# Optimization experiments

Measured on AMD Instinct MI355X. Metric: run time of the kernel, lower is better.

Reference implementation:

```python
import jax, jax.numpy as jnp
import numpy as np

B, IN_C, OUT_C, NUM, DIM = 4096, 512, 512, 16, 128

def _unif(k, shape, fan_in):
    b = 1.0 / np.sqrt(fan_in)
    return jax.random.uniform(k, shape, jnp.float32, -b, b)

def setup_inputs() -> dict:
    key = jax.random.key(0)
    ks = jax.random.split(key, 9)
    inp = jax.random.normal(ks[0], (B, IN_C), jnp.float32)
    Wpre = _unif(ks[1], (DIM, IN_C), IN_C)        # nn.Linear weight (out, in)
    bpre = _unif(ks[2], (DIM,), IN_C)
    W = _unif(ks[3], (NUM, NUM, DIM, DIM), DIM)    # W[i,j] = link[i][j].weight (out=e, in=d)
    bl = _unif(ks[4], (NUM, NUM, DIM), DIM)        # link biases
    life = jax.random.uniform(ks[5], (NUM, NUM), jnp.float32) + 0.5  # rand(1)+0.5
    Wpost = _unif(ks[6], (OUT_C, DIM), DIM)
    bpost = _unif(ks[7], (OUT_C,), DIM)
    return {"inp": inp, "Wpre": Wpre, "bpre": bpre, "W": W, "b": bl,
            "life": life, "Wpost": Wpost, "bpost": bpost, "steps": 10}

def reference(inp, Wpre, bpre, W, b, life, Wpost, bpost, steps):
    num = life.shape[0]
    x = inp @ Wpre.T + bpre                         # [B, dim]
    gate = jnp.where(life > 0, life, 0.0)           # life>0 branch with scalar gain
    Wg = gate[:, :, None, None] * W                 # [num, num, dim, dim]
    bias = jnp.einsum('ij,ijd->jd', gate, b)        # per-step constant bias sum over i
    m0 = jnp.zeros((num,) + x.shape, x.dtype).at[0].set(x)  # matrix[0] = inp
    def step(m, _):
        # new[j] = sum_i gate[i,j] * (m[i] @ W[i,j].T + b[i,j])
        new = jnp.einsum('ibd,ijed->jbe', m, Wg) + bias[:, None, :]
        return new, None
    mT, _ = jax.lax.scan(step, m0, None, length=steps)
    return mT[num - 1] @ Wpost.T + bpost            # [B, out_c]
```

## Files before the change

### kernel.cpp

```cpp
#include <hip/hip_runtime.h>


typedef __bf16 bf16x8 __attribute__((ext_vector_type(8)));
typedef float f32x4 __attribute__((ext_vector_type(4)));
typedef __attribute__((address_space(3))) unsigned int lds_u32;
typedef const __attribute__((address_space(1))) unsigned int glb_u32;

__device__ __forceinline__ unsigned short f2bf(float x) {
  unsigned int u = __float_as_uint(x);
  u += 0x7FFFu + ((u >> 16) & 1u);
  return (unsigned short)(u >> 16);
}
__device__ __forceinline__ float bf2f(unsigned short s) {
  return __uint_as_float(((unsigned int)s) << 16);
}
__device__ __forceinline__ bf16x8 ldg8(const unsigned short* p) {
  return __builtin_bit_cast(bf16x8, *(const uint4*)p);
}
__device__ __forceinline__ f32x4 mfma16(bf16x8 a, bf16x8 b, f32x4 c) {
  return __builtin_amdgcn_mfma_f32_16x16x32_bf16(a, b, c, 0, 0, 0);
}

#define ND 2048
#define MT 144
#define KS 8
#define CKS 16

__global__ __launch_bounds__(256) void build_all(
    const float* __restrict__ W, const float* __restrict__ life,
    const float* __restrict__ bl, const float* __restrict__ inp,
    unsigned short* __restrict__ Ahi, unsigned short* __restrict__ Alo,
    unsigned short* __restrict__ Qhi, unsigned short* __restrict__ Qlo,
    unsigned short* __restrict__ Rhi, unsigned short* __restrict__ Rlo,
    float* __restrict__ beta,
    unsigned short* __restrict__ Ihi, unsigned short* __restrict__ Ilo) {
  const int tid = blockIdx.x * 256 + threadIdx.x;
  const int NT = gridDim.x * 256;

  for (int item = tid; item < (ND * ND) / 8; item += NT) {
    int base = item * 8;
    int n = base >> 11, k = base & 2047;
    int j = n >> 7, i = k >> 7;
    float gval = life[i * 16 + j];
    float gate = gval > 0.f ? gval : 0.f;
    const float* src = W + ((i * 16 + j) * 16384 + (n & 127) * 128 + (k & 127));
    float4 x = *(const float4*)src, y = *(const float4*)(src + 4);
    float vals[8] = {x.x, x.y, x.z, x.w, y.x, y.y, y.z, y.w};
    union { unsigned short u[8]; uint4 v; } ph, pl;
#pragma unroll
    for (int q = 0; q < 8; ++q) {
      float v = gate * vals[q];
      unsigned short h = f2bf(v);
      ph.u[q] = h;
      pl.u[q] = f2bf(v - bf2f(h));
    }
    *(uint4*)(Ahi + base) = ph.v;
    *(uint4*)(Alo + base) = pl.v;
  }

  for (int item = tid; item < MT * ND; item += NT) {
    int m = item >> 11, n = item & 2047;
    int j = n >> 7, e = n & 127;
    unsigned short hh = 0, ll = 0;
    if (m < 128) {
      float gval = life[j];
      float gate = gval > 0.f ? gval : 0.f;
      float v = gate * W[j * 16384 + e * 128 + m];
      hh = f2bf(v); ll = f2bf(v - bf2f(hh));
    } else if (m == 128) {
      float s = 0.f;
#pragma unroll
      for (int i = 0; i < 16; ++i) {
        float gval = life[i * 16 + j];
        float gate = gval > 0.f ? gval : 0.f;
        s += gate * bl[(i * 16 + j) * 128 + e];
      }
      beta[n] = s;
      hh = f2bf(s); ll = f2bf(s - bf2f(hh));
    }
    Qhi[item] = hh;
    Qlo[item] = ll;
  }

  for (int item = tid; item < MT * ND; item += NT) {
    int m = item >> 11, n = item & 2047;
    int i = n >> 7, d = n & 127;
    unsigned short hh = 0, ll = 0;
    if (m < 128) {
      float gval = life[i * 16 + 15];
      float gate = gval > 0.f ? gval : 0.f;
      float v = gate * W[(i * 16 + 15) * 16384 + m * 128 + d];
      hh = f2bf(v); ll = f2bf(v - bf2f(hh));
    }
    Rhi[item] = hh;
    Rlo[item] = ll;
  }

  for (int item = tid; item < (4096 * 512) / 8; item += NT) {
    int base = item * 8;
    float4 x = *(const float4*)(inp + base), y = *(const float4*)(inp + base + 4);
    float vals[8] = {x.x, x.y, x.z, x.w, y.x, y.y, y.z, y.w};
    union { unsigned short u[8]; uint4 v; } ph, pl;
#pragma unroll
    for (int q = 0; q < 8; ++q) {
      unsigned short h = f2bf(vals[q]);
      ph.u[q] = h;
      pl.u[q] = f2bf(vals[q] - bf2f(h));
    }
    *(uint4*)(Ihi + base) = ph.v;
    *(uint4*)(Ilo + base) = pl.v;
  }
}

__global__ __launch_bounds__(256) void build_AT(
    const unsigned short* __restrict__ Ahi, const unsigned short* __restrict__ Alo,
    unsigned short* __restrict__ AThi, unsigned short* __restrict__ ATlo) {
  __shared__ unsigned short Th[32][36], Tl[32][36];
  const int t = threadIdx.x;
  const int tx = blockIdx.x & 63;
  const int ty = blockIdx.x >> 6;
  const int r = t >> 3;
  const int c4 = (t & 7) * 4;
  union { uint2 d; unsigned short u[4]; } vh, vl;
  vh.d = *(const uint2*)(Ahi + (size_t)(tx * 32 + r) * ND + ty * 32 + c4);
  vl.d = *(const uint2*)(Alo + (size_t)(tx * 32 + r) * ND + ty * 32 + c4);
#pragma unroll
  for (int i = 0; i < 4; ++i) { Th[r][c4 + i] = vh.u[i]; Tl[r][c4 + i] = vl.u[i]; }
  __syncthreads();
  union { uint2 d; unsigned short u[4]; } oh, ol;
#pragma unroll
  for (int i = 0; i < 4; ++i) { oh.u[i] = Th[c4 + i][r]; ol.u[i] = Tl[c4 + i][r]; }
  *(uint2*)(AThi + (size_t)(ty * 32 + r) * ND + tx * 32 + c4) = oh.d;
  *(uint2*)(ATlo + (size_t)(ty * 32 + r) * ND + tx * 32 + c4) = ol.d;
}

__global__ __launch_bounds__(192, 2) void step_pair(
    const unsigned short* __restrict__ Ahi, const unsigned short* __restrict__ Alo,
    const unsigned short* __restrict__ AThi, const unsigned short* __restrict__ ATlo,
    const unsigned short* __restrict__ Qqhi, const unsigned short* __restrict__ Qqlo,
    const unsigned short* __restrict__ Qrhi, const unsigned short* __restrict__ Qrlo,
    float* __restrict__ Pq, float* __restrict__ Pr) {
  __shared__ __align__(16) unsigned short AS[64][256];
  const int t = threadIdx.x;
  const int g = t >> 6, lane = t & 63;
  const int r16 = lane & 15, q = lane >> 4;
  const int kc = blockIdx.x;
  const int nb = blockIdx.y;
  const int chain = blockIdx.z;
  const unsigned short* Bh = chain ? AThi : Ahi;
  const unsigned short* Bl = chain ? ATlo : Alo;
  const unsigned short* Qh = chain ? Qrhi : Qqhi;
  const unsigned short* Ql = chain ? Qrlo : Qqlo;
  float* P = chain ? Pr : Pq;
  const int kbase = kc * 256;
  const int n0 = nb * 32;

  for (int ch = g; ch < 32; ch += 3) {
    int s = ch * 64 + lane;
    int row = s >> 5;
    int c16 = (s & 31) ^ (row & 7);
    const unsigned short* src =
        (row < 32 ? Bh + (size_t)(n0 + row) * ND
                  : Bl + (size_t)(n0 + row - 32) * ND) + kbase + c16 * 8;
    __builtin_amdgcn_global_load_lds((glb_u32*)src,
                                     (lds_u32*)(&AS[0][0] + ch * 512), 16, 0, 0);
  }

  const int m0 = g * 48 + r16;
  const unsigned short* pA0h = Qh + (size_t)m0 * ND + kbase + q * 8;
  const unsigned short* pA0l = Ql + (size_t)m0 * ND + kbase + q * 8;

  bf16x8 qa[2][6];
#pragma unroll
  for (int f = 0; f < 3; ++f) {
    qa[0][2 * f]     = ldg8(pA0h + f * 16 * ND);
    qa[0][2 * f + 1] = ldg8(pA0l + f * 16 * ND);
  }
  __syncthreads();

  const uint4* ASv = (const uint4*)&AS[0][0];

  f32x4 acc[3][2];
#pragma unroll
  for (int mt = 0; mt < 3; ++mt)
#pragma unroll
    for (int nt = 0; nt < 2; ++nt) acc[mt][nt] = (f32x4){0.f, 0.f, 0.f, 0.f};

#pragma unroll
  for (int it = 0; it < 8; ++it) {
    const int cur = it & 1, nxt = cur ^ 1;
    if (it < 7) {
      const int ko = (it + 1) * 32;
#pragma unroll
      for (int f = 0; f < 3; ++f) {
        qa[nxt][2 * f]     = ldg8(pA0h + f * 16 * ND + ko);
        qa[nxt][2 * f + 1] = ldg8(pA0l + f * 16 * ND + ko);
      }
    }
    const int cx = (it * 4 + q) ^ (r16 & 7);
    bf16x8 b0h = __builtin_bit_cast(bf16x8, ASv[r16 * 32 + cx]);
    bf16x8 b1h = __builtin_bit_cast(bf16x8, ASv[(16 + r16) * 32 + cx]);
    bf16x8 b0l = __builtin_bit_cast(bf16x8, ASv[(32 + r16) * 32 + cx]);
    bf16x8 b1l = __builtin_bit_cast(bf16x8, ASv[(48 + r16) * 32 + cx]);

    acc[0][0] = mfma16(qa[cur][0], b0h, acc[0][0]);
    acc[0][0] = mfma16(qa[cur][1], b0h, acc[0][0]);
    acc[0][0] = mfma16(qa[cur][0], b0l, acc[0][0]);
    acc[1][0] = mfma16(qa[cur][2], b0h, acc[1][0]);
    acc[1][0] = mfma16(qa[cur][3], b0h, acc[1][0]);
    acc[1][0] = mfma16(qa[cur][2], b0l, acc[1][0]);
    acc[2][0] = mfma16(qa[cur][4], b0h, acc[2][0]);
    acc[2][0] = mfma16(qa[cur][5], b0h, acc[2][0]);
    acc[2][0] = mfma16(qa[cur][4], b0l, acc[2][0]);
    acc[0][1] = mfma16(qa[cur][0], b1h, acc[0][1]);
    acc[0][1] = mfma16(qa[cur][1], b1h, acc[0][1]);
    acc[0][1] = mfma16(qa[cur][0], b1l, acc[0][1]);
    acc[1][1] = mfma16(qa[cur][2], b1h, acc[1][1]);
    acc[1][1] = mfma16(qa[cur][3], b1h, acc[1][1]);
    acc[1][1] = mfma16(qa[cur][2], b1l, acc[1][1]);
    acc[2][1] = mfma16(qa[cur][4], b1h, acc[2][1]);
    acc[2][1] = mfma16(qa[cur][5], b1h, acc[2][1]);
    acc[2][1] = mfma16(qa[cur][4], b1l, acc[2][1]);
  }

  float* Pk = P + kc * (MT * ND);
#pragma unroll
  for (int mt = 0; mt < 3; ++mt)
#pragma unroll
    for (int nt = 0; nt < 2; ++nt) {
      int mbase = g * 48 + mt * 16 + q * 4;
      int n = n0 + nt * 16 + r16;
#pragma unroll
      for (int r = 0; r < 4; ++r)
        Pk[(mbase + r) * ND + n] = acc[mt][nt][r];
    }
}

__global__ __launch_bounds__(256) void reduce_pair(
    const float* __restrict__ Pq, const float* __restrict__ Pr,
    const float* __restrict__ beta,
    unsigned short* __restrict__ Oqh, unsigned short* __restrict__ Oql,
    unsigned short* __restrict__ Orh, unsigned short* __restrict__ Orl) {
  int bid = blockIdx.x;
  int chain = bid >= 288;
  int t = (bid - (chain ? 288 : 0)) * 256 + threadIdx.x;
  const float* P = chain ? Pr : Pq;
  unsigned short* Oh = chain ? Orh : Oqh;
  unsigned short* Ol = chain ? Orl : Oql;
  int m = t >> 9;
  int n = (t & 511) * 4;
  int idx = m * ND + n;
  const int stride = MT * ND;
  float v0 = 0.f, v1 = 0.f, v2 = 0.f, v3 = 0.f;
#pragma unroll
  for (int c = 0; c < KS; ++c) {
    float4 s = *(const float4*)(P + c * stride + idx);
    v0 += s.x; v1 += s.y; v2 += s.z; v3 += s.w;
  }
  if (!chain && m == 128) {
    float4 b4 = *(const float4*)(beta + n);
    v0 += b4.x; v1 += b4.y; v2 += b4.z; v3 += b4.w;
  }
  union { unsigned short u[4]; uint2 d; } h, l;
  float vv[4] = {v0, v1, v2, v3};
#pragma unroll
  for (int i = 0; i < 4; ++i) {
    unsigned short hh = f2bf(vv[i]);
    h.u[i] = hh;
    l.u[i] = f2bf(vv[i] - bf2f(hh));
  }
  *(uint2*)(Oh + idx) = h.d;
  *(uint2*)(Ol + idx) = l.d;
}

__global__ __launch_bounds__(192, 2) void contract_S(
    const unsigned short* __restrict__ R5h, const unsigned short* __restrict__ R5l,
    const unsigned short* __restrict__ Q5h, const unsigned short* __restrict__ Q5l,
    float* __restrict__ CP) {
  __shared__ __align__(16) unsigned short AS[64][128];
  const int t = threadIdx.x;
  const int g = t >> 6, lane = t & 63;
  const int r16 = lane & 15, q = lane >> 4;
  const int kc = blockIdx.x;
  const int nb = blockIdx.y;
  const int kbase = kc * 128;
  const int n0 = nb * 32;

  for (int ch = g; ch < 16; ch += 3) {
    int s = ch * 64 + lane;
    int row = s >> 4;
    int c16 = (s & 15) ^ (row & 7);
    const unsigned short* src =
        (row < 32 ? R5h + (size_t)(n0 + row) * ND
                  : R5l + (size_t)(n0 + row - 32) * ND) + kbase + c16 * 8;
    __builtin_amdgcn_global_load_lds((glb_u32*)src,
                                     (lds_u32*)(&AS[0][0] + ch * 512), 16, 0, 0);
  }

  const int m0 = g * 48 + r16;
  const unsigned short* pA0h = Q5h + (size_t)m0 * ND + kbase + q * 8;
  const unsigned short* pA0l = Q5l + (size_t)m0 * ND + kbase + q * 8;

  bf16x8 qa[2][6];
#pragma unroll
  for (int f = 0; f < 3; ++f) {
    qa[0][2 * f]     = ldg8(pA0h + f * 16 * ND);
    qa[0][2 * f + 1] = ldg8(pA0l + f * 16 * ND);
  }
  __syncthreads();

  const uint4* ASv = (const uint4*)&AS[0][0];

  f32x4 acc[3][2];
#pragma unroll
  for (int mt = 0; mt < 3; ++mt)
#pragma unroll
    for (int nt = 0; nt < 2; ++nt) acc[mt][nt] = (f32x4){0.f, 0.f, 0.f, 0.f};

#pragma unroll
  for (int it = 0; it < 4; ++it) {
    const int cur = it & 1, nxt = cur ^ 1;
    if (it < 3) {
      const int ko = (it + 1) * 32;
#pragma unroll
      for (int f = 0; f < 3; ++f) {
        qa[nxt][2 * f]     = ldg8(pA0h + f * 16 * ND + ko);
        qa[nxt][2 * f + 1] = ldg8(pA0l + f * 16 * ND + ko);
      }
    }
    const int cx = (it * 4 + q) ^ (r16 & 7);
    bf16x8 b0h = __builtin_bit_cast(bf16x8, ASv[r16 * 16 + cx]);
    bf16x8 b1h = __builtin_bit_cast(bf16x8, ASv[(16 + r16) * 16 + cx]);
    bf16x8 b0l = __builtin_bit_cast(bf16x8, ASv[(32 + r16) * 16 + cx]);
    bf16x8 b1l = __builtin_bit_cast(bf16x8, ASv[(48 + r16) * 16 + cx]);

    acc[0][0] = mfma16(qa[cur][0], b0h, acc[0][0]);
    acc[0][0] = mfma16(qa[cur][1], b0h, acc[0][0]);
    acc[0][0] = mfma16(qa[cur][0], b0l, acc[0][0]);
    acc[1][0] = mfma16(qa[cur][2], b0h, acc[1][0]);
    acc[1][0] = mfma16(qa[cur][3], b0h, acc[1][0]);
    acc[1][0] = mfma16(qa[cur][2], b0l, acc[1][0]);
    acc[2][0] = mfma16(qa[cur][4], b0h, acc[2][0]);
    acc[2][0] = mfma16(qa[cur][5], b0h, acc[2][0]);
    acc[2][0] = mfma16(qa[cur][4], b0l, acc[2][0]);
    acc[0][1] = mfma16(qa[cur][0], b1h, acc[0][1]);
    acc[0][1] = mfma16(qa[cur][1], b1h, acc[0][1]);
    acc[0][1] = mfma16(qa[cur][0], b1l, acc[0][1]);
    acc[1][1] = mfma16(qa[cur][2], b1h, acc[1][1]);
    acc[1][1] = mfma16(qa[cur][3], b1h, acc[1][1]);
    acc[1][1] = mfma16(qa[cur][2], b1l, acc[1][1]);
    acc[2][1] = mfma16(qa[cur][4], b1h, acc[2][1]);
    acc[2][1] = mfma16(qa[cur][5], b1h, acc[2][1]);
    acc[2][1] = mfma16(qa[cur][4], b1l, acc[2][1]);
  }

  float* Pk = CP + kc * (MT * 128);
#pragma unroll
  for (int mt = 0; mt < 3; ++mt)
#pragma unroll
    for (int nt = 0; nt < 2; ++nt) {
      int mbase = g * 48 + mt * 16 + q * 4;
      int n = n0 + nt * 16 + r16;
#pragma unroll
      for (int r = 0; r < 4; ++r)
        Pk[(mbase + r) * 128 + n] = acc[mt][nt][r];
    }
}

__global__ __launch_bounds__(256) void extract_Sc(
    const float* __restrict__ CP,
    const unsigned short* __restrict__ Q5h, const unsigned short* __restrict__ Q5l,
    float* __restrict__ St, float* __restrict__ gv) {
  int t = blockIdx.x * 256 + threadIdx.x;
  const int PSTR = MT * 128;
  if (t < 16384) {
    int d = t >> 7, e = t & 127;
    float v = 0.f;
#pragma unroll
    for (int c = 0; c < CKS; ++c) v += CP[c * PSTR + d * 128 + e];
    St[t] = v;
  } else if (t < 16512) {
    int e = t - 16384;
    float v = bf2f(Q5h[128 * ND + 1920 + e]) + bf2f(Q5l[128 * ND + 1920 + e]);
#pragma unroll
    for (int c = 0; c < CKS; ++c) v += CP[c * PSTR + 128 * 128 + e];
    gv[e] = v;
  }
}

__global__ __launch_bounds__(256) void tail_T1g(
    const float* __restrict__ St, const float* __restrict__ Wpre,
    const float* __restrict__ bpre, float* __restrict__ T1,
    float* __restrict__ gv) {
  int t = blockIdx.x * 256 + threadIdx.x;
  if (t < 65536) {
    int e = t >> 9, ic = t & 511;
    float s = 0.f;
    for (int d = 0; d < 128; ++d) s += St[d * 128 + e] * Wpre[d * 512 + ic];
    T1[t] = s;
  } else if (t < 65664) {
    int e = t - 65536;
    float s = gv[e];
    for (int d = 0; d < 128; ++d) s += St[d * 128 + e] * bpre[d];
    gv[e] = s;
  }
}

__global__ __launch_bounds__(256) void tail_Weff(
    const float* __restrict__ Wpost, const float* __restrict__ T1,
    const float* __restrict__ gv, const float* __restrict__ bpost,
    unsigned short* __restrict__ Whi, unsigned short* __restrict__ Wlo,
    float* __restrict__ beff) {
  int t = blockIdx.x * 256 + threadIdx.x;
  if (t < 262144) {
    int o = t >> 9, ic = t & 511;
    float s = 0.f;
    for (int e = 0; e < 128; ++e) s += Wpost[o * 128 + e] * T1[e * 512 + ic];
    unsigned short h = f2bf(s);
    Whi[t] = h;
    Wlo[t] = f2bf(s - bf2f(h));
  } else if (t < 262656) {
    int o = t - 262144;
    float s = bpost[o];
    for (int e = 0; e < 128; ++e) s += Wpost[o * 128 + e] * gv[e];
    beff[o] = s;
  }
}

__global__ __launch_bounds__(256) void final_gemm(
    const unsigned short* __restrict__ Ihi, const unsigned short* __restrict__ Ilo,
    const unsigned short* __restrict__ Whi, const unsigned short* __restrict__ Wlo,
    const float* __restrict__ beff, float* __restrict__ out) {
  __shared__ __align__(16) unsigned short Is_hi[64][40], Is_lo[64][40];
  __shared__ __align__(16) unsigned short Ws_hi[128][40], Ws_lo[128][40];
  const int t = threadIdx.x;
  const int mb = blockIdx.x, nb = blockIdx.y;
  const int w = t >> 6, lane = t & 63;
  const int r16 = lane & 15, q = lane >> 4;

  f32x4 acc[4][2];
#pragma unroll
  for (int x = 0; x < 4; ++x)
#pragma unroll
    for (int b = 0; b < 2; ++b) acc[x][b] = (f32x4){0.f, 0.f, 0.f, 0.f};

  for (int kc = 0; kc < 16; ++kc) {
    const int k0 = kc * 32;
#pragma unroll
    for (int rpt = 0; rpt < 6; ++rpt) {
      int slot = t + rpt * 256;
      if (slot < 512) {
        int arr = slot >> 8, s = slot & 255;
        int row = s >> 2, off = (s & 3) * 8;
        const unsigned short* src = arr ? Ilo : Ihi;
        unsigned short* dst = arr ? &Is_lo[row][off] : &Is_hi[row][off];
        *(uint4*)dst = *(const uint4*)(src + (mb * 64 + row) * 512 + k0 + off);
      } else {
        int s = slot - 512;
        int arr = s >> 9, s2 = s & 511;
        int row = s2 >> 2, off = (s2 & 3) * 8;
        const unsigned short* src = arr ? Wlo : Whi;
        unsigned short* dst = arr ? &Ws_lo[row][off] : &Ws_hi[row][off];
        *(uint4*)dst = *(const uint4*)(src + (nb * 128 + row) * 512 + k0 + off);
      }
    }
    __syncthreads();

    bf16x8 bh0 = __builtin_bit_cast(bf16x8, *(const uint4*)&Ws_hi[w * 32 + r16][q * 8]);
    bf16x8 bl0 = __builtin_bit_cast(bf16x8, *(const uint4*)&Ws_lo[w * 32 + r16][q * 8]);
    bf16x8 bh1 = __builtin_bit_cast(bf16x8, *(const uint4*)&Ws_hi[w * 32 + 16 + r16][q * 8]);
    bf16x8 bl1 = __builtin_bit_cast(bf16x8, *(const uint4*)&Ws_lo[w * 32 + 16 + r16][q * 8]);
#pragma unroll
    for (int mt = 0; mt < 4; ++mt) {
      bf16x8 ah = __builtin_bit_cast(bf16x8, *(const uint4*)&Is_hi[mt * 16 + r16][q * 8]);
      bf16x8 al = __builtin_bit_cast(bf16x8, *(const uint4*)&Is_lo[mt * 16 + r16][q * 8]);
      acc[mt][0] = mfma16(ah, bh0, acc[mt][0]);
      acc[mt][0] = mfma16(al, bh0, acc[mt][0]);
      acc[mt][0] = mfma16(ah, bl0, acc[mt][0]);
      acc[mt][1] = mfma16(ah, bh1, acc[mt][1]);
      acc[mt][1] = mfma16(al, bh1, acc[mt][1]);
      acc[mt][1] = mfma16(ah, bl1, acc[mt][1]);
    }
    __syncthreads();
  }

#pragma unroll
  for (int mt = 0; mt < 4; ++mt)
#pragma unroll
    for (int nt = 0; nt < 2; ++nt) {
      int n = nb * 128 + w * 32 + nt * 16 + r16;
      float bv = beff[n];
#pragma unroll
      for (int r = 0; r < 4; ++r) {
        int m = mb * 64 + mt * 16 + q * 4 + r;
        out[m * 512 + n] = acc[mt][nt][r] + bv;
      }
    }
}

extern "C" void kernel_launch(void* const* d_in, const int* in_sizes, int n_in,
                              void* d_out, int out_size, void* d_ws, size_t ws_size,
                              hipStream_t stream) {
  const float* inp   = (const float*)d_in[0];
  const float* Wpre  = (const float*)d_in[1];
  const float* bpre  = (const float*)d_in[2];
  const float* W     = (const float*)d_in[3];
  const float* bl    = (const float*)d_in[4];
  const float* life  = (const float*)d_in[5];
  const float* Wpost = (const float*)d_in[6];
  const float* bpost = (const float*)d_in[7];
  float* out = (float*)d_out;

  char* p = (char*)d_ws;
  auto alloc = [&](size_t bytes) {
    char* r = p;
    p += (bytes + 255) & ~(size_t)255;
    return r;
  };
  unsigned short* Ahi  = (unsigned short*)alloc((size_t)ND * ND * 2);
  unsigned short* Alo  = (unsigned short*)alloc((size_t)ND * ND * 2);
  unsigned short* AThi = (unsigned short*)alloc((size_t)ND * ND * 2);
  unsigned short* ATlo = (unsigned short*)alloc((size_t)ND * ND * 2);
  unsigned short* QqAh = (unsigned short*)alloc((size_t)MT * ND * 2);
  unsigned short* QqAl = (unsigned short*)alloc((size_t)MT * ND * 2);
  unsigned short* QqBh = (unsigned short*)alloc((size_t)MT * ND * 2);
  unsigned short* QqBl = (unsigned short*)alloc((size_t)MT * ND * 2);
  unsigned short* QrAh = (unsigned short*)alloc((size_t)MT * ND * 2);
  unsigned short* QrAl = (unsigned short*)alloc((size_t)MT * ND * 2);
  unsigned short* QrBh = (unsigned short*)alloc((size_t)MT * ND * 2);
  unsigned short* QrBl = (unsigned short*)alloc((size_t)MT * ND * 2);
  float* beta = (float*)alloc(ND * 4);
  float* Pq   = (float*)alloc((size_t)KS * MT * ND * 4);
  float* Pr   = (float*)alloc((size_t)KS * MT * ND * 4);
  float* CP   = (float*)alloc((size_t)CKS * MT * 128 * 4);
  float* St   = (float*)alloc(128 * 128 * 4);
  float* gv   = (float*)alloc(128 * 4);
  float* T1   = (float*)alloc(128 * 512 * 4);
  float* beff = (float*)alloc(512 * 4);
  unsigned short* Whi = (unsigned short*)alloc(512 * 512 * 2);
  unsigned short* Wlo = (unsigned short*)alloc(512 * 512 * 2);
  unsigned short* Ihi = (unsigned short*)alloc((size_t)4096 * 512 * 2);
  unsigned short* Ilo = (unsigned short*)alloc((size_t)4096 * 512 * 2);

  build_all<<<1024, 256, 0, stream>>>(W, life, bl, inp, Ahi, Alo,
                                      QqAh, QqAl, QrAh, QrAl, beta, Ihi, Ilo);
  build_AT<<<4096, 256, 0, stream>>>(Ahi, Alo, AThi, ATlo);

  const unsigned short *qqh = QqAh, *qql = QqAl, *qrh = QrAh, *qrl = QrAl;
  unsigned short *oqh = QqBh, *oql = QqBl, *orh = QrBh, *orl = QrBl;
  for (int s = 0; s < 4; ++s) {
    step_pair<<<dim3(KS, 64, 2), 192, 0, stream>>>(
        Ahi, Alo, AThi, ATlo, qqh, qql, qrh, qrl, Pq, Pr);
    reduce_pair<<<576, 256, 0, stream>>>(Pq, Pr, beta, oqh, oql, orh, orl);
    const unsigned short* t1 = qqh; qqh = oqh; oqh = (unsigned short*)t1;
    const unsigned short* t2 = qql; qql = oql; oql = (unsigned short*)t2;
    const unsigned short* t3 = qrh; qrh = orh; orh = (unsigned short*)t3;
    const unsigned short* t4 = qrl; qrl = orl; orl = (unsigned short*)t4;
  }

  contract_S<<<dim3(CKS, 4), 192, 0, stream>>>(qrh, qrl, qqh, qql, CP);
  extract_Sc<<<65, 256, 0, stream>>>(CP, qqh, qql, St, gv);
  tail_T1g<<<257, 256, 0, stream>>>(St, Wpre, bpre, T1, gv);
  tail_Weff<<<1026, 256, 0, stream>>>(Wpost, T1, gv, bpost, Whi, Wlo, beff);
  final_gemm<<<dim3(64, 4), 256, 0, stream>>>(Ihi, Ilo, Whi, Wlo, beff, out);
}
```

Before: 254.0 us.

## Fuse A transpose into build kernel and double-buffer final GEMM LDS tiles

The separate build_AT kernel is removed. build_all now produces both A and its transpose from the same register values through a shared-memory tile, so the second pass that re-read A from global memory and the extra launch disappear. Separately, final_gemm stages the next K chunk in registers while the current chunk is being multiplied, using double-buffered LDS so global loads overlap with MFMA work. The cost is more LDS and register pressure in final_gemm and extra block-wide barriers inside build_all's tile loop.

```diff
diff --git a/kernel.cpp b/kernel.cpp
--- a/kernel.cpp
+++ b/kernel.cpp
@@ -30,32 +30,49 @@
     const float* __restrict__ W, const float* __restrict__ life,
     const float* __restrict__ bl, const float* __restrict__ inp,
     unsigned short* __restrict__ Ahi, unsigned short* __restrict__ Alo,
+    unsigned short* __restrict__ AThi, unsigned short* __restrict__ ATlo,
     unsigned short* __restrict__ Qhi, unsigned short* __restrict__ Qlo,
     unsigned short* __restrict__ Rhi, unsigned short* __restrict__ Rlo,
     float* __restrict__ beta,
     unsigned short* __restrict__ Ihi, unsigned short* __restrict__ Ilo) {
+  __shared__ unsigned short Th[32][36], Tl[32][36];
   const int tid = blockIdx.x * 256 + threadIdx.x;
   const int NT = gridDim.x * 256;
-
-  for (int item = tid; item < (ND * ND) / 8; item += NT) {
-    int base = item * 8;
-    int n = base >> 11, k = base & 2047;
-    int j = n >> 7, i = k >> 7;
-    float gval = life[i * 16 + j];
-    float gate = gval > 0.f ? gval : 0.f;
-    const float* src = W + ((i * 16 + j) * 16384 + (n & 127) * 128 + (k & 127));
-    float4 x = *(const float4*)src, y = *(const float4*)(src + 4);
-    float vals[8] = {x.x, x.y, x.z, x.w, y.x, y.y, y.z, y.w};
-    union { unsigned short u[8]; uint4 v; } ph, pl;
-#pragma unroll
-    for (int q = 0; q < 8; ++q) {
-      float v = gate * vals[q];
-      unsigned short h = f2bf(v);
-      ph.u[q] = h;
-      pl.u[q] = f2bf(v - bf2f(h));
-    }
-    *(uint4*)(Ahi + base) = ph.v;
-    *(uint4*)(Alo + base) = pl.v;
+  const int t = threadIdx.x;
+
+  {
+    const int r = t >> 3;
+    const int c4 = (t & 7) * 4;
+    for (int tt = blockIdx.x; tt < 4096; tt += gridDim.x) {
+      int nt = tt & 63, kt = tt >> 6;
+      int j = nt >> 2, e0 = (nt & 3) * 32;
+      int i = kt >> 2, d0 = (kt & 3) * 32;
+      float gval = life[i * 16 + j];
+      float gate = gval > 0.f ? gval : 0.f;
+      const float* src = W + ((size_t)(i * 16 + j) * 16384 + (e0 + r) * 128 + d0 + c4);
+      float4 v = *(const float4*)src;
+      float vals[4] = {v.x, v.y, v.z, v.w};
+      union { unsigned short u[4]; uint2 d2; } oh, ol;
+#pragma unroll
+      for (int x = 0; x < 4; ++x) {
+        float s = gate * vals[x];
+        oh.u[x] = f2bf(s);
+        ol.u[x] = f2bf(s - bf2f(oh.u[x]));
+      }
+      size_t aidx = (size_t)(j * 128 + e0 + r) * ND + i * 128 + d0 + c4;
+      *(uint2*)(Ahi + aidx) = oh.d2;
+      *(uint2*)(Alo + aidx) = ol.d2;
+      __syncthreads();
+#pragma unroll
+      for (int x = 0; x < 4; ++x) { Th[r][c4 + x] = oh.u[x]; Tl[r][c4 + x] = ol.u[x]; }
+      __syncthreads();
+      union { unsigned short u[4]; uint2 d2; } th, tl;
+#pragma unroll
+      for (int x = 0; x < 4; ++x) { th.u[x] = Th[c4 + x][r]; tl.u[x] = Tl[c4 + x][r]; }
+      size_t tidx = (size_t)(i * 128 + d0 + r) * ND + j * 128 + e0 + c4;
+      *(uint2*)(AThi + tidx) = th.d2;
+      *(uint2*)(ATlo + tidx) = tl.d2;
+    }
   }
 
   for (int item = tid; item < MT * ND; item += NT) {
@@ -89,7 +106,7 @@
     if (m < 128) {
       float gval = life[i * 16 + 15];
       float gate = gval > 0.f ? gval : 0.f;
-      float v = gate * W[(i * 16 + 15) * 16384 + m * 128 + d];
+      float v = gate * W[(size_t)(i * 16 + 15) * 16384 + m * 128 + d];
       hh = f2bf(v); ll = f2bf(v - bf2f(hh));
     }
     Rhi[item] = hh;
@@ -110,28 +127,6 @@
     *(uint4*)(Ihi + base) = ph.v;
     *(uint4*)(Ilo + base) = pl.v;
   }
-}
-
-__global__ __launch_bounds__(256) void build_AT(
-    const unsigned short* __restrict__ Ahi, const unsigned short* __restrict__ Alo,
-    unsigned short* __restrict__ AThi, unsigned short* __restrict__ ATlo) {
-  __shared__ unsigned short Th[32][36], Tl[32][36];
-  const int t = threadIdx.x;
-  const int tx = blockIdx.x & 63;
-  const int ty = blockIdx.x >> 6;
-  const int r = t >> 3;
-  const int c4 = (t & 7) * 4;
-  union { uint2 d; unsigned short u[4]; } vh, vl;
-  vh.d = *(const uint2*)(Ahi + (size_t)(tx * 32 + r) * ND + ty * 32 + c4);
-  vl.d = *(const uint2*)(Alo + (size_t)(tx * 32 + r) * ND + ty * 32 + c4);
-#pragma unroll
-  for (int i = 0; i < 4; ++i) { Th[r][c4 + i] = vh.u[i]; Tl[r][c4 + i] = vl.u[i]; }
-  __syncthreads();
-  union { uint2 d; unsigned short u[4]; } oh, ol;
-#pragma unroll
-  for (int i = 0; i < 4; ++i) { oh.u[i] = Th[c4 + i][r]; ol.u[i] = Tl[c4 + i][r]; }
-  *(uint2*)(AThi + (size_t)(ty * 32 + r) * ND + tx * 32 + c4) = oh.d;
-  *(uint2*)(ATlo + (size_t)(ty * 32 + r) * ND + tx * 32 + c4) = ol.d;
 }
 
 __global__ __launch_bounds__(192, 2) void step_pair(
@@ -431,20 +426,15 @@
     const unsigned short* __restrict__ Ihi, const unsigned short* __restrict__ Ilo,
     const unsigned short* __restrict__ Whi, const unsigned short* __restrict__ Wlo,
     const float* __restrict__ beff, float* __restrict__ out) {
-  __shared__ __align__(16) unsigned short Is_hi[64][40], Is_lo[64][40];
-  __shared__ __align__(16) unsigned short Ws_hi[128][40], Ws_lo[128][40];
+  __shared__ __align__(16) unsigned short Is_hi[2][64][40], Is_lo[2][64][40];
+  __shared__ __align__(16) unsigned short Ws_hi[2][128][40], Ws_lo[2][128][40];
   const int t = threadIdx.x;
   const int mb = blockIdx.x, nb = blockIdx.y;
   const int w = t >> 6, lane = t & 63;
   const int r16 = lane & 15, q = lane >> 4;
 
-  f32x4 acc[4][2];
-#pragma unroll
-  for (int x = 0; x < 4; ++x)
-#pragma unroll
-    for (int b = 0; b < 2; ++b) acc[x][b] = (f32x4){0.f, 0.f, 0.f, 0.f};
-
-  for (int kc = 0; kc < 16; ++kc) {
+  uint4 stg[6];
+  auto load_regs = [&](int kc) {
     const int k0 = kc * 32;
 #pragma unroll
     for (int rpt = 0; rpt < 6; ++rpt) {
@@ -453,27 +443,57 @@
         int arr = slot >> 8, s = slot & 255;
         int row = s >> 2, off = (s & 3) * 8;
         const unsigned short* src = arr ? Ilo : Ihi;
-        unsigned short* dst = arr ? &Is_lo[row][off] : &Is_hi[row][off];
-        *(uint4*)dst = *(const uint4*)(src + (mb * 64 + row) * 512 + k0 + off);
+        stg[rpt] = *(const uint4*)(src + (mb * 64 + row) * 512 + k0 + off);
       } else {
         int s = slot - 512;
         int arr = s >> 9, s2 = s & 511;
         int row = s2 >> 2, off = (s2 & 3) * 8;
         const unsigned short* src = arr ? Wlo : Whi;
-        unsigned short* dst = arr ? &Ws_lo[row][off] : &Ws_hi[row][off];
-        *(uint4*)dst = *(const uint4*)(src + (nb * 128 + row) * 512 + k0 + off);
-      }
-    }
-    __syncthreads();
-
-    bf16x8 bh0 = __builtin_bit_cast(bf16x8, *(const uint4*)&Ws_hi[w * 32 + r16][q * 8]);
-    bf16x8 bl0 = __builtin_bit_cast(bf16x8, *(const uint4*)&Ws_lo[w * 32 + r16][q * 8]);
-    bf16x8 bh1 = __builtin_bit_cast(bf16x8, *(const uint4*)&Ws_hi[w * 32 + 16 + r16][q * 8]);
-    bf16x8 bl1 = __builtin_bit_cast(bf16x8, *(const uint4*)&Ws_lo[w * 32 + 16 + r16][q * 8]);
+        stg[rpt] = *(const uint4*)(src + (nb * 128 + row) * 512 + k0 + off);
+      }
+    }
+  };
+  auto store_lds = [&](int b) {
+#pragma unroll
+    for (int rpt = 0; rpt < 6; ++rpt) {
+      int slot = t + rpt * 256;
+      if (slot < 512) {
+        int arr = slot >> 8, s = slot & 255;
+        int row = s >> 2, off = (s & 3) * 8;
+        unsigned short* dst = arr ? &Is_lo[b][row][off] : &Is_hi[b][row][off];
+        *(uint4*)dst = stg[rpt];
+      } else {
+        int s = slot - 512;
+        int arr = s >> 9, s2 = s & 511;
+        int row = s2 >> 2, off = (s2 & 3) * 8;
+        unsigned short* dst = arr ? &Ws_lo[b][row][off] : &Ws_hi[b][row][off];
+        *(uint4*)dst = stg[rpt];
+      }
+    }
+  };
+
+  f32x4 acc[4][2];
+#pragma unroll
+  for (int x = 0; x < 4; ++x)
+#pragma unroll
+    for (int b = 0; b < 2; ++b) acc[x][b] = (f32x4){0.f, 0.f, 0.f, 0.f};
+
+  load_regs(0);
+  store_lds(0);
+  __syncthreads();
+
+  for (int kc = 0; kc < 16; ++kc) {
+    const int cur = kc & 1;
+    if (kc < 15) load_regs(kc + 1);
+
+    bf16x8 bh0 = __builtin_bit_cast(bf16x8, *(const uint4*)&Ws_hi[cur][w * 32 + r16][q * 8]);
+    bf16x8 bl0 = __builtin_bit_cast(bf16x8, *(const uint4*)&Ws_lo[cur][w * 32 + r16][q * 8]);
+    bf16x8 bh1 = __builtin_bit_cast(bf16x8, *(const uint4*)&Ws_hi[cur][w * 32 + 16 + r16][q * 8]);
+    bf16x8 bl1 = __builtin_bit_cast(bf16x8, *(const uint4*)&Ws_lo[cur][w * 32 + 16 + r16][q * 8]);
 #pragma unroll
     for (int mt = 0; mt < 4; ++mt) {
-      bf16x8 ah = __builtin_bit_cast(bf16x8, *(const uint4*)&Is_hi[mt * 16 + r16][q * 8]);
-      bf16x8 al = __builtin_bit_cast(bf16x8, *(const uint4*)&Is_lo[mt * 16 + r16][q * 8]);
+      bf16x8 ah = __builtin_bit_cast(bf16x8, *(const uint4*)&Is_hi[cur][mt * 16 + r16][q * 8]);
+      bf16x8 al = __builtin_bit_cast(bf16x8, *(const uint4*)&Is_lo[cur][mt * 16 + r16][q * 8]);
       acc[mt][0] = mfma16(ah, bh0, acc[mt][0]);
       acc[mt][0] = mfma16(al, bh0, acc[mt][0]);
       acc[mt][0] = mfma16(ah, bl0, acc[mt][0]);
@@ -481,6 +501,8 @@
       acc[mt][1] = mfma16(al, bh1, acc[mt][1]);
       acc[mt][1] = mfma16(ah, bl1, acc[mt][1]);
     }
+
+    if (kc < 15) store_lds(cur ^ 1);
     __syncthreads();
   }
 
@@ -542,9 +564,8 @@
   unsigned short* Ihi = (unsigned short*)alloc((size_t)4096 * 512 * 2);
   unsigned short* Ilo = (unsigned short*)alloc((size_t)4096 * 512 * 2);
 
-  build_all<<<1024, 256, 0, stream>>>(W, life, bl, inp, Ahi, Alo,
+  build_all<<<1024, 256, 0, stream>>>(W, life, bl, inp, Ahi, Alo, AThi, ATlo,
                                       QqAh, QqAl, QrAh, QrAl, beta, Ihi, Ilo);
-  build_AT<<<4096, 256, 0, stream>>>(Ahi, Alo, AThi, ATlo);
 
   const unsigned short *qqh = QqAh, *qql = QqAl, *qrh = QrAh, *qrl = QrAl;
   unsigned short *oqh = QqBh, *oql = QqBl, *orh = QrBh, *orl = QrBl;
```

New measurement: 323.1 us. +27.2%, slower.
